# Performance work log

Measured on AMD Instinct MI355X. Metric: run time of the kernel, lower is better.

Reference implementation:

```python
import jax, jax.numpy as jnp
import numpy as np

N_NODES = 50000

def gcn_conv(x, W, b, row, col, ew, n):
    # PyG GCNConv: linear first (no bias in lin), then gcn_norm with added
    # self-loops (weight 1.0), symmetric D^{-1/2} normalization, scatter-add
    # aggregation from row (source) to col (target), then bias.
    h = x @ W                                      # [N, out]
    loop = jnp.arange(n, dtype=row.dtype)
    row_f = jnp.concatenate([row, loop])
    col_f = jnp.concatenate([col, loop])
    ew_f = jnp.concatenate([ew, jnp.ones((n,), dtype=ew.dtype)])
    deg = jax.ops.segment_sum(ew_f, col_f, num_segments=n)
    dinv = jnp.where(deg > 0, jax.lax.rsqrt(jnp.maximum(deg, 1e-30)), 0.0)
    norm = dinv[row_f] * ew_f * dinv[col_f]        # [E+N]
    msg = norm[:, None] * h[row_f]                 # gather + scale
    out = jax.ops.segment_sum(msg, col_f, num_segments=n)  # scatter-add
    return out + b

def setup_inputs() -> dict:
    key = jax.random.key(0)
    k = jax.random.split(key, 8)
    in_dim, hidden_dim, out_dim = 128, 256, 128
    n, e = N_NODES, 600000
    x = jax.random.normal(k[0], (n, in_dim), dtype=jnp.float32)
    edge_index = jax.random.randint(k[1], (2, e), 0, n, dtype=jnp.int64)
    edge_weight = jax.random.uniform(k[2], (e,), dtype=jnp.float32)
    # Glorot-style params (PyG GCNConv lin has no bias; bias added after aggregation)
    W1 = jax.random.normal(k[3], (in_dim, hidden_dim), dtype=jnp.float32) / np.sqrt(in_dim)
    b1 = jnp.zeros((hidden_dim,), dtype=jnp.float32)
    W2 = jax.random.normal(k[4], (hidden_dim, out_dim), dtype=jnp.float32) / np.sqrt(hidden_dim)
    b2 = jnp.zeros((out_dim,), dtype=jnp.float32)
    return {"x": x, "edge_index": edge_index, "edge_weight": edge_weight,
            "W1": W1, "b1": b1, "W2": W2, "b2": b2}

def reference(x, edge_index, edge_weight, W1, b1, W2, b2):
    n = x.shape[0]
    row, col = edge_index[0], edge_index[1]
    h = jax.nn.relu(gcn_conv(x, W1, b1, row, col, edge_weight, n))
    # dropout is identity in eval mode
    out = jax.nn.relu(gcn_conv(h, W2, b2, row, col, edge_weight, n))
    return out
```

## Files before the change

kernel.cpp:

```cpp
#include <hip/hip_runtime.h>
#include <hip/hip_bf16.h>

constexpr int IN_DIM  = 128;
constexpr int HID     = 256;
constexpr int OUT_DIM = 128;
constexpr int ELL_W   = 64;

typedef __attribute__((ext_vector_type(8))) short short8;
typedef __attribute__((ext_vector_type(8))) unsigned short ushort8;
typedef __attribute__((ext_vector_type(4))) float f32x4;

__device__ __forceinline__ float bf2f(unsigned short u) {
    return __uint_as_float(((unsigned int)u) << 16);
}
__device__ __forceinline__ unsigned short f2bf(float f) {
    unsigned int u = __float_as_uint(f);
    u += 0x7FFFu + ((u >> 16) & 1u);
    return (unsigned short)(u >> 16);
}
__device__ __forceinline__ unsigned short f2h(float f) {
    _Float16 h = (_Float16)f;
    unsigned short b;
    __builtin_memcpy(&b, &h, 2);
    return b;
}
__device__ __forceinline__ float h2f(unsigned short b) {
    _Float16 h;
    __builtin_memcpy(&h, &b, 2);
    return (float)h;
}
__device__ __forceinline__ unsigned int pack_e(int src, float w) {
    return (unsigned int)src | ((unsigned int)f2h(w) << 16);
}

__device__ __forceinline__ void ell_gather_acc(
    const unsigned int* __restrict__ bucket, int m,
    const unsigned short* __restrict__ tab, int j8, int gw, int l16,
    float acc[8]) {
    for (int base = 0; base < m; base += 16) {
        const unsigned int mt = (base + l16 < m) ? bucket[base + l16] : 0u;
        const int c16   = min(m - base, 16);
        const int pairs = (c16 + 1) >> 1;
        unsigned int u0 = __shfl(mt, gw * 16 + 0);
        unsigned int u1 = __shfl(mt, gw * 16 + 1);
        ushort8 v0 = *(const ushort8*)&tab[(size_t)(u0 & 0xFFFFu) * 128 + j8];
        ushort8 v1 = *(const ushort8*)&tab[(size_t)(u1 & 0xFFFFu) * 128 + j8];
        for (int p = 1; p < pairs; ++p) {
            const unsigned int n0 = __shfl(mt, gw * 16 + 2 * p);
            const unsigned int n1 = __shfl(mt, gw * 16 + 2 * p + 1);
            const ushort8 w0 = *(const ushort8*)&tab[(size_t)(n0 & 0xFFFFu) * 128 + j8];
            const ushort8 w1 = *(const ushort8*)&tab[(size_t)(n1 & 0xFFFFu) * 128 + j8];
            const float f0 = h2f((unsigned short)(u0 >> 16));
            const float f1 = h2f((unsigned short)(u1 >> 16));
            #pragma unroll
            for (int i = 0; i < 8; ++i) acc[i] = fmaf(f0, bf2f(v0[i]), acc[i]);
            #pragma unroll
            for (int i = 0; i < 8; ++i) acc[i] = fmaf(f1, bf2f(v1[i]), acc[i]);
            u0 = n0; u1 = n1; v0 = w0; v1 = w1;
        }
        const float f0 = h2f((unsigned short)(u0 >> 16));
        const float f1 = h2f((unsigned short)(u1 >> 16));
        #pragma unroll
        for (int i = 0; i < 8; ++i) acc[i] = fmaf(f0, bf2f(v0[i]), acc[i]);
        #pragma unroll
        for (int i = 0; i < 8; ++i) acc[i] = fmaf(f1, bf2f(v1[i]), acc[i]);
    }
}

__global__ void k_prep(int* __restrict__ cnt, int n,
                       const float* __restrict__ W1, unsigned short* __restrict__ w1t,
                       const float* __restrict__ W2, unsigned short* __restrict__ w2t) {
    const int i = blockIdx.x * 256 + threadIdx.x;
    if (i < n) cnt[i] = 0;
    if (i < IN_DIM * HID) {
        const int k = i / HID, nn = i % HID;
        w1t[(size_t)nn * IN_DIM + k] = f2bf(W1[i]);
    }
    if (i < HID * OUT_DIM) {
        const int k = i / OUT_DIM, nn = i % OUT_DIM;
        w2t[(size_t)nn * HID + k] = f2bf(W2[i]);
    }
}

__global__ void k_fill_ell(const int* __restrict__ row, const int* __restrict__ col,
                           const float* __restrict__ ew, int* __restrict__ cnt,
                           unsigned int* __restrict__ ell, int E) {
    const int i  = blockIdx.x * blockDim.x + threadIdx.x;
    const int e0 = i * 4;
    if (e0 + 3 < E) {
        const int4   c4 = *reinterpret_cast<const int4*>(col + e0);
        const int4   r4 = *reinterpret_cast<const int4*>(row + e0);
        const float4 w4 = *reinterpret_cast<const float4*>(ew + e0);
        const int p0 = atomicAdd(&cnt[c4.x], 1);
        const int p1 = atomicAdd(&cnt[c4.y], 1);
        const int p2 = atomicAdd(&cnt[c4.z], 1);
        const int p3 = atomicAdd(&cnt[c4.w], 1);
        if (p0 < ELL_W) ell[(size_t)c4.x * ELL_W + p0] = pack_e(r4.x, w4.x);
        if (p1 < ELL_W) ell[(size_t)c4.y * ELL_W + p1] = pack_e(r4.y, w4.y);
        if (p2 < ELL_W) ell[(size_t)c4.z * ELL_W + p2] = pack_e(r4.z, w4.z);
        if (p3 < ELL_W) ell[(size_t)c4.w * ELL_W + p3] = pack_e(r4.w, w4.w);
    } else {
        for (int e = e0; e < E; ++e) {
            const int c = col[e];
            const int p = atomicAdd(&cnt[c], 1);
            if (p < ELL_W) ell[(size_t)c * ELL_W + p] = pack_e(row[e], ew[e]);
        }
    }
}

__global__ __launch_bounds__(256)
void k_deg_xs(const int* __restrict__ cnt, const unsigned int* __restrict__ ell,
              const float* __restrict__ x, float* __restrict__ dinv,
              unsigned short* __restrict__ xs, int n) {
    const int wave = threadIdx.x >> 6;
    const int lane = threadIdx.x & 63;
    const int node = blockIdx.x * 4 + wave;
    if (node >= n) return;
    const int m = min(cnt[node], ELL_W);
    float s = (lane < m) ? h2f((unsigned short)(ell[(size_t)node * ELL_W + lane] >> 16)) : 0.f;
    #pragma unroll
    for (int d = 32; d; d >>= 1) s += __shfl_xor(s, d);
    const float di = rsqrtf(1.0f + s);
    if (lane == 0) dinv[node] = di;
    const float2 v = *reinterpret_cast<const float2*>(x + (size_t)node * IN_DIM + lane * 2);
    const unsigned int packed = (unsigned int)f2bf(v.x * di) |
                                ((unsigned int)f2bf(v.y * di) << 16);
    *reinterpret_cast<unsigned int*>(xs + (size_t)node * IN_DIM + lane * 2) = packed;
}

template<bool BIAS_RELU, bool BF16OUT>
__global__ __launch_bounds__(256)
void k_gather_w(const int* __restrict__ cnt, const unsigned int* __restrict__ ell,
                const float* __restrict__ dinv, const unsigned short* __restrict__ hs,
                const float* __restrict__ bias, void* __restrict__ out_, int n) {
    constexpr int F = 128;
    const int gid  = threadIdx.x >> 4;
    const int gw   = gid & 3;
    const int l16  = threadIdx.x & 15;
    const int j8   = l16 * 8;
    const int node = blockIdx.x * 16 + gid;
    if (node >= n) return;

    const int m = min(cnt[node], ELL_W);
    const unsigned int* bucket = ell + (size_t)node * ELL_W;

    float acc[8] = {};
    ell_gather_acc(bucket, m, hs, j8, gw, l16, acc);

    const float dc = dinv[node];
    const ushort8 hv = *reinterpret_cast<const ushort8*>(hs + (size_t)node * F + j8);
    float o[8];
    if (BIAS_RELU) {
        const float4 b0 = *reinterpret_cast<const float4*>(bias + j8);
        const float4 b1 = *reinterpret_cast<const float4*>(bias + j8 + 4);
        const float bb[8] = {b0.x, b0.y, b0.z, b0.w, b1.x, b1.y, b1.z, b1.w};
        #pragma unroll
        for (int i = 0; i < 8; ++i)
            o[i] = fmaxf(fmaf(dc, acc[i] + bf2f(hv[i]), bb[i]), 0.f);
    } else {
        #pragma unroll
        for (int i = 0; i < 8; ++i) o[i] = dc * (acc[i] + bf2f(hv[i]));
    }
    if (BF16OUT) {
        unsigned short ob[8];
        #pragma unroll
        for (int i = 0; i < 8; ++i) ob[i] = f2bf(o[i]);
        *reinterpret_cast<uint4*>((unsigned short*)out_ + (size_t)node * F + j8) =
            *reinterpret_cast<uint4*>(ob);
    } else {
        float* op = (float*)out_ + (size_t)node * F + j8;
        *reinterpret_cast<float4*>(op)     = make_float4(o[0], o[1], o[2], o[3]);
        *reinterpret_cast<float4*>(op + 4) = make_float4(o[4], o[5], o[6], o[7]);
    }
}

__global__ __launch_bounds__(256)
void k_fused_gemm(const int* __restrict__ cnt, const unsigned int* __restrict__ ell,
                  const float* __restrict__ dinv, const unsigned short* __restrict__ xs,
                  const unsigned short* __restrict__ W1t,
                  const unsigned short* __restrict__ W2t,
                  const float* __restrict__ b1,
                  unsigned short* __restrict__ H2,
                  int n) {
    __shared__ unsigned short As2[64 * 128];
    __shared__ unsigned short Bs [256 * 64];
    __shared__ unsigned short Hs [64 * 256];

    const int t    = threadIdx.x;
    const int w    = t >> 6;
    const int lane = t & 63;
    const int quad = lane >> 4;
    const int l16  = lane & 15;
    const int lrow = lane >> 3;
    const int lcol = ((lane & 7) ^ lrow) * 8;
    const int xr   = (l16 & 7) << 3;
    const int rowBase = blockIdx.x * 64;

    const unsigned short* gB1 = W1t + (size_t)(w * 64 + lrow) * IN_DIM + lcol;
    const unsigned short* gB2 = W2t + (size_t)(w * 32 + lrow) * HID + lcol;

    auto stageW1 = [&](unsigned short* buf, int k0) {
        #pragma unroll
        for (int j = 0; j < 8; ++j)
            __builtin_amdgcn_global_load_lds(
                (const __attribute__((address_space(1))) uint32_t*)(gB1 + k0 + (size_t)j * 8 * IN_DIM),
                (__attribute__((address_space(3))) uint32_t*)(&buf[(w * 64 + j * 8) * 64]), 16, 0, 0);
    };
    auto stageW2 = [&](unsigned short* buf, int k0) {
        #pragma unroll
        for (int j = 0; j < 4; ++j)
            __builtin_amdgcn_global_load_lds(
                (const __attribute__((address_space(1))) uint32_t*)(gB2 + k0 + (size_t)j * 8 * HID),
                (__attribute__((address_space(3))) uint32_t*)(&buf[(w * 32 + j * 8) * 64]), 16, 0, 0);
    };

    stageW1(Bs, 0);

    {
        const int gid = t >> 4;
        const int gw  = gid & 3;
        const int j8  = l16 * 8;
        for (int it = 0; it < 4; ++it) {
            const int r    = gid * 4 + it;
            const int node = rowBase + r;
            const int xw   = (r & 7) << 3;
            if (node < n) {
                const int m = min(cnt[node], ELL_W);
                const unsigned int* bucket = ell + (size_t)node * ELL_W;
                float acc[8] = {};
                ell_gather_acc(bucket, m, xs, j8, gw, l16, acc);
                const float dc = dinv[node];
                const ushort8 hv = *reinterpret_cast<const ushort8*>(xs + (size_t)node * IN_DIM + j8);
                unsigned short ob[8];
                #pragma unroll
                for (int i = 0; i < 8; ++i) ob[i] = f2bf(dc * (acc[i] + bf2f(hv[i])));
                *reinterpret_cast<uint4*>(&As2[r * 128 + (j8 ^ xw)]) = *reinterpret_cast<uint4*>(ob);
            } else {
                uint4 z = {0u, 0u, 0u, 0u};
                *reinterpret_cast<uint4*>(&As2[r * 128 + (j8 ^ xw)]) = z;
            }
        }
    }

    f32x4 acc[4][4] = {};
    auto mma1 = [&](const unsigned short* Bbuf, int k0) {
        #pragma unroll
        for (int ks = 0; ks < 2; ++ks) {
            short8 af[4], bfr[4];
            #pragma unroll
            for (int mt = 0; mt < 4; ++mt)
                af[mt] = *(const short8*)&As2[(mt * 16 + l16) * 128 + ((k0 + ks * 32 + quad * 8) ^ xr)];
            #pragma unroll
            for (int nt = 0; nt < 4; ++nt)
                bfr[nt] = *(const short8*)&Bbuf[(w * 64 + nt * 16 + l16) * 64 + ((ks * 32 + quad * 8) ^ xr)];
            #pragma unroll
            for (int mt = 0; mt < 4; ++mt)
                #pragma unroll
                for (int nt = 0; nt < 4; ++nt)
                    acc[mt][nt] = __builtin_amdgcn_mfma_f32_16x16x32_bf16(
                        af[mt], bfr[nt], acc[mt][nt], 0, 0, 0);
        }
    };

    __syncthreads();
    stageW1(Hs, 64);
    mma1(Bs, 0);
    __syncthreads();
    mma1(Hs, 64);
    __syncthreads();

    stageW2(As2, 0);

    {
        float bv[4];
        #pragma unroll
        for (int nt = 0; nt < 4; ++nt) bv[nt] = b1[w * 64 + nt * 16 + l16];
        #pragma unroll
        for (int mt = 0; mt < 4; ++mt)
            #pragma unroll
            for (int i = 0; i < 4; ++i) {
                const int row = mt * 16 + quad * 4 + i;
                const int xw  = (row & 7) << 3;
                #pragma unroll
                for (int nt = 0; nt < 4; ++nt) {
                    const int col = w * 64 + nt * 16 + l16;
                    Hs[row * 256 + (col ^ xw)] = f2bf(fmaxf(acc[mt][nt][i] + bv[nt], 0.f));
                }
            }
    }

    f32x4 acc2[4][2] = {};
    auto mma2 = [&](const unsigned short* Bbuf, int k0) {
        #pragma unroll
        for (int ks = 0; ks < 2; ++ks) {
            short8 af[4], bfr[2];
            #pragma unroll
            for (int mt = 0; mt < 4; ++mt)
                af[mt] = *(const short8*)&Hs[(mt * 16 + l16) * 256 + ((k0 + ks * 32 + quad * 8) ^ xr)];
            #pragma unroll
            for (int nt = 0; nt < 2; ++nt)
                bfr[nt] = *(const short8*)&Bbuf[(w * 32 + nt * 16 + l16) * 64 + ((ks * 32 + quad * 8) ^ xr)];
            #pragma unroll
            for (int mt = 0; mt < 4; ++mt)
                #pragma unroll
                for (int nt = 0; nt < 2; ++nt)
                    acc2[mt][nt] = __builtin_amdgcn_mfma_f32_16x16x32_bf16(
                        af[mt], bfr[nt], acc2[mt][nt], 0, 0, 0);
        }
    };

    __syncthreads();
    stageW2(Bs, 64);
    mma2(As2, 0);
    __syncthreads();
    stageW2(As2, 128);
    mma2(Bs, 64);
    __syncthreads();
    stageW2(Bs, 192);
    mma2(As2, 128);
    __syncthreads();
    mma2(Bs, 192);

    #pragma unroll
    for (int mt = 0; mt < 4; ++mt)
        #pragma unroll
        for (int i = 0; i < 4; ++i) {
            const int r = rowBase + mt * 16 + quad * 4 + i;
            if (r < n) {
                const float dr = dinv[r];
                #pragma unroll
                for (int nt = 0; nt < 2; ++nt) {
                    const int c = w * 32 + nt * 16 + l16;
                    H2[(size_t)r * OUT_DIM + c] = f2bf(acc2[mt][nt][i] * dr);
                }
            }
        }
}

extern "C" void kernel_launch(void* const* d_in, const int* in_sizes, int n_in,
                              void* d_out, int out_size, void* d_ws, size_t ws_size,
                              hipStream_t stream) {
    const float* x  = (const float*)d_in[0];
    const int*   ei = (const int*)d_in[1];
    const float* ew = (const float*)d_in[2];
    const float* W1 = (const float*)d_in[3];
    const float* b1 = (const float*)d_in[4];
    const float* W2 = (const float*)d_in[5];
    const float* b2 = (const float*)d_in[6];
    float* out = (float*)d_out;

    const int n = in_sizes[0] / IN_DIM;
    const int E = in_sizes[1] / 2;
    const int Mpad = (n + 127) & ~127;
    const int* row = ei;
    const int* col = ei + E;

    float* ws = (float*)d_ws;
    size_t o = 0;
    auto alloc = [&](size_t words) { float* p = ws + o; o += (words + 63) & ~(size_t)63; return p; };
    float* dinv = alloc(n);
    int*   cnt  = (int*)alloc(n);
    unsigned int* ell = (unsigned int*)alloc((size_t)n * ELL_W);
    unsigned short* xs   = (unsigned short*)alloc((size_t)Mpad * IN_DIM / 2);
    unsigned short* h2s  = (unsigned short*)alloc((size_t)Mpad * OUT_DIM / 2);
    unsigned short* w1t  = (unsigned short*)alloc((size_t)IN_DIM * HID / 2);
    unsigned short* w2t  = (unsigned short*)alloc((size_t)HID * OUT_DIM / 2);

    k_prep<<<(n + 255) / 256, 256, 0, stream>>>(cnt, n, W1, w1t, W2, w2t);
    k_fill_ell<<<(E / 4 + 255) / 256, 256, 0, stream>>>(row, col, ew, cnt, ell, E);
    k_deg_xs<<<(n + 3) / 4, 256, 0, stream>>>(cnt, ell, x, dinv, xs, n);

    k_fused_gemm<<<Mpad / 64, 256, 0, stream>>>(cnt, ell, dinv, xs, w1t, w2t, b1, h2s, n);

    k_gather_w<true, false><<<(n + 15) / 16, 256, 0, stream>>>(cnt, ell, dinv, h2s, b2, out, n);
}
```

Measured before the change: 210.9 us.

## Split layer-1 aggregation out of fused GEMM and compute degree via atomics

Moves the first-layer ELL gather out of the fused GEMM kernel into a separate k_gather_w launch that writes aggregated bf16 features to a new buffer. The GEMM kernel then stages its A tile straight from global memory with async LDS loads. Node degree is now accumulated with float atomics during the ELL fill, replacing the per-node wave reduction in k_deg_xs. This aims to give the gather its own higher-occupancy launch and avoid gather latency stalls inside the LDS-heavy GEMM blocks. In exchange it adds an extra global round trip of the aggregated features, one more kernel launch, and extra atomics on the edge fill.

```diff
diff --git a/kernel.cpp b/kernel.cpp
--- a/kernel.cpp
+++ b/kernel.cpp
@@ -67,11 +67,11 @@
     }
 }
 
-__global__ void k_prep(int* __restrict__ cnt, int n,
+__global__ void k_prep(int* __restrict__ cnt, float* __restrict__ deg, int n,
                        const float* __restrict__ W1, unsigned short* __restrict__ w1t,
                        const float* __restrict__ W2, unsigned short* __restrict__ w2t) {
     const int i = blockIdx.x * 256 + threadIdx.x;
-    if (i < n) cnt[i] = 0;
+    if (i < n) { cnt[i] = 0; deg[i] = 0.f; }
     if (i < IN_DIM * HID) {
         const int k = i / HID, nn = i % HID;
         w1t[(size_t)nn * IN_DIM + k] = f2bf(W1[i]);
@@ -84,7 +84,7 @@
 
 __global__ void k_fill_ell(const int* __restrict__ row, const int* __restrict__ col,
                            const float* __restrict__ ew, int* __restrict__ cnt,
-                           unsigned int* __restrict__ ell, int E) {
+                           float* __restrict__ deg, unsigned int* __restrict__ ell, int E) {
     const int i  = blockIdx.x * blockDim.x + threadIdx.x;
     const int e0 = i * 4;
     if (e0 + 3 < E) {
@@ -95,6 +95,10 @@
         const int p1 = atomicAdd(&cnt[c4.y], 1);
         const int p2 = atomicAdd(&cnt[c4.z], 1);
         const int p3 = atomicAdd(&cnt[c4.w], 1);
+        atomicAdd(&deg[c4.x], w4.x);
+        atomicAdd(&deg[c4.y], w4.y);
+        atomicAdd(&deg[c4.z], w4.z);
+        atomicAdd(&deg[c4.w], w4.w);
         if (p0 < ELL_W) ell[(size_t)c4.x * ELL_W + p0] = pack_e(r4.x, w4.x);
         if (p1 < ELL_W) ell[(size_t)c4.y * ELL_W + p1] = pack_e(r4.y, w4.y);
         if (p2 < ELL_W) ell[(size_t)c4.z * ELL_W + p2] = pack_e(r4.z, w4.z);
@@ -103,24 +107,20 @@
         for (int e = e0; e < E; ++e) {
             const int c = col[e];
             const int p = atomicAdd(&cnt[c], 1);
+            atomicAdd(&deg[c], ew[e]);
             if (p < ELL_W) ell[(size_t)c * ELL_W + p] = pack_e(row[e], ew[e]);
         }
     }
 }
 
 __global__ __launch_bounds__(256)
-void k_deg_xs(const int* __restrict__ cnt, const unsigned int* __restrict__ ell,
-              const float* __restrict__ x, float* __restrict__ dinv,
-              unsigned short* __restrict__ xs, int n) {
+void k_deg_xs(const float* __restrict__ deg, const float* __restrict__ x,
+              float* __restrict__ dinv, unsigned short* __restrict__ xs, int n) {
     const int wave = threadIdx.x >> 6;
     const int lane = threadIdx.x & 63;
     const int node = blockIdx.x * 4 + wave;
     if (node >= n) return;
-    const int m = min(cnt[node], ELL_W);
-    float s = (lane < m) ? h2f((unsigned short)(ell[(size_t)node * ELL_W + lane] >> 16)) : 0.f;
-    #pragma unroll
-    for (int d = 32; d; d >>= 1) s += __shfl_xor(s, d);
-    const float di = rsqrtf(1.0f + s);
+    const float di = rsqrtf(1.0f + deg[node]);
     if (lane == 0) dinv[node] = di;
     const float2 v = *reinterpret_cast<const float2*>(x + (size_t)node * IN_DIM + lane * 2);
     const unsigned int packed = (unsigned int)f2bf(v.x * di) |
@@ -175,14 +175,14 @@
 }
 
 __global__ __launch_bounds__(256)
-void k_fused_gemm(const int* __restrict__ cnt, const unsigned int* __restrict__ ell,
-                  const float* __restrict__ dinv, const unsigned short* __restrict__ xs,
-                  const unsigned short* __restrict__ W1t,
-                  const unsigned short* __restrict__ W2t,
-                  const float* __restrict__ b1,
-                  unsigned short* __restrict__ H2,
-                  int n) {
-    __shared__ unsigned short As2[64 * 128];
+void k_gemm_dual(const unsigned short* __restrict__ A,
+                 const unsigned short* __restrict__ W1t,
+                 const unsigned short* __restrict__ W2t,
+                 const float* __restrict__ b1,
+                 const float* __restrict__ dinv,
+                 unsigned short* __restrict__ H2,
+                 int n) {
+    __shared__ unsigned short As[64 * 128];
     __shared__ unsigned short Bs [256 * 64];
     __shared__ unsigned short Hs [64 * 256];
 
@@ -199,6 +199,17 @@
     const unsigned short* gB1 = W1t + (size_t)(w * 64 + lrow) * IN_DIM + lcol;
     const unsigned short* gB2 = W2t + (size_t)(w * 32 + lrow) * HID + lcol;
 
+    auto stageA = [&]() {
+        #pragma unroll
+        for (int j = 0; j < 4; ++j) {
+            const int ci = w * 64 + j * 256 + lane;
+            const int r  = ci >> 4;
+            const int c  = (lane & 15) ^ (r & 7);
+            __builtin_amdgcn_global_load_lds(
+                (const __attribute__((address_space(1))) uint32_t*)(A + (size_t)(rowBase + r) * 128 + c * 8),
+                (__attribute__((address_space(3))) uint32_t*)(&As[(size_t)ci * 8]), 16, 0, 0);
+        }
+    };
     auto stageW1 = [&](unsigned short* buf, int k0) {
         #pragma unroll
         for (int j = 0; j < 8; ++j)
@@ -214,34 +225,6 @@
                 (__attribute__((address_space(3))) uint32_t*)(&buf[(w * 32 + j * 8) * 64]), 16, 0, 0);
     };
 
-    stageW1(Bs, 0);
-
-    {
-        const int gid = t >> 4;
-        const int gw  = gid & 3;
-        const int j8  = l16 * 8;
-        for (int it = 0; it < 4; ++it) {
-            const int r    = gid * 4 + it;
-            const int node = rowBase + r;
-            const int xw   = (r & 7) << 3;
-            if (node < n) {
-                const int m = min(cnt[node], ELL_W);
-                const unsigned int* bucket = ell + (size_t)node * ELL_W;
-                float acc[8] = {};
-                ell_gather_acc(bucket, m, xs, j8, gw, l16, acc);
-                const float dc = dinv[node];
-                const ushort8 hv = *reinterpret_cast<const ushort8*>(xs + (size_t)node * IN_DIM + j8);
-                unsigned short ob[8];
-                #pragma unroll
-                for (int i = 0; i < 8; ++i) ob[i] = f2bf(dc * (acc[i] + bf2f(hv[i])));
-                *reinterpret_cast<uint4*>(&As2[r * 128 + (j8 ^ xw)]) = *reinterpret_cast<uint4*>(ob);
-            } else {
-                uint4 z = {0u, 0u, 0u, 0u};
-                *reinterpret_cast<uint4*>(&As2[r * 128 + (j8 ^ xw)]) = z;
-            }
-        }
-    }
-
     f32x4 acc[4][4] = {};
     auto mma1 = [&](const unsigned short* Bbuf, int k0) {
         #pragma unroll
@@ -249,7 +232,7 @@
             short8 af[4], bfr[4];
             #pragma unroll
             for (int mt = 0; mt < 4; ++mt)
-                af[mt] = *(const short8*)&As2[(mt * 16 + l16) * 128 + ((k0 + ks * 32 + quad * 8) ^ xr)];
+                af[mt] = *(const short8*)&As[(mt * 16 + l16) * 128 + ((k0 + ks * 32 + quad * 8) ^ xr)];
             #pragma unroll
             for (int nt = 0; nt < 4; ++nt)
                 bfr[nt] = *(const short8*)&Bbuf[(w * 64 + nt * 16 + l16) * 64 + ((ks * 32 + quad * 8) ^ xr)];
@@ -262,6 +245,8 @@
         }
     };
 
+    stageA();
+    stageW1(Bs, 0);
     __syncthreads();
     stageW1(Hs, 64);
     mma1(Bs, 0);
@@ -269,7 +254,7 @@
     mma1(Hs, 64);
     __syncthreads();
 
-    stageW2(As2, 0);
+    stageW2(As, 0);
 
     {
         float bv[4];
@@ -311,13 +296,13 @@
 
     __syncthreads();
     stageW2(Bs, 64);
-    mma2(As2, 0);
-    __syncthreads();
-    stageW2(As2, 128);
+    mma2(As, 0);
+    __syncthreads();
+    stageW2(As, 128);
     mma2(Bs, 64);
     __syncthreads();
     stageW2(Bs, 192);
-    mma2(As2, 128);
+    mma2(As, 128);
     __syncthreads();
     mma2(Bs, 192);
 
@@ -359,18 +344,22 @@
     size_t o = 0;
     auto alloc = [&](size_t words) { float* p = ws + o; o += (words + 63) & ~(size_t)63; return p; };
     float* dinv = alloc(n);
+    float* deg  = alloc(n);
     int*   cnt  = (int*)alloc(n);
     unsigned int* ell = (unsigned int*)alloc((size_t)n * ELL_W);
     unsigned short* xs   = (unsigned short*)alloc((size_t)Mpad * IN_DIM / 2);
+    unsigned short* aggx = (unsigned short*)alloc((size_t)Mpad * IN_DIM / 2);
     unsigned short* h2s  = (unsigned short*)alloc((size_t)Mpad * OUT_DIM / 2);
     unsigned short* w1t  = (unsigned short*)alloc((size_t)IN_DIM * HID / 2);
     unsigned short* w2t  = (unsigned short*)alloc((size_t)HID * OUT_DIM / 2);
 
-    k_prep<<<(n + 255) / 256, 256, 0, stream>>>(cnt, n, W1, w1t, W2, w2t);
-    k_fill_ell<<<(E / 4 + 255) / 256, 256, 0, stream>>>(row, col, ew, cnt, ell, E);
-    k_deg_xs<<<(n + 3) / 4, 256, 0, stream>>>(cnt, ell, x, dinv, xs, n);
-
-    k_fused_gemm<<<Mpad / 64, 256, 0, stream>>>(cnt, ell, dinv, xs, w1t, w2t, b1, h2s, n);
+    k_prep<<<(n + 255) / 256, 256, 0, stream>>>(cnt, deg, n, W1, w1t, W2, w2t);
+    k_fill_ell<<<(E / 4 + 255) / 256, 256, 0, stream>>>(row, col, ew, cnt, deg, ell, E);
+    k_deg_xs<<<(n + 3) / 4, 256, 0, stream>>>(deg, x, dinv, xs, n);
+
+    k_gather_w<false, true><<<(n + 15) / 16, 256, 0, stream>>>(cnt, ell, dinv, xs, nullptr, aggx, n);
+
+    k_gemm_dual<<<Mpad / 64, 256, 0, stream>>>(aggx, w1t, w2t, b1, dinv, h2s, n);
 
     k_gather_w<true, false><<<(n + 15) / 16, 256, 0, stream>>>(cnt, ell, dinv, h2s, b2, out, n);
 }
```

New measurement: 229.6 us. 8.9% more time.
